# Optimization experiments

Measured on AMD Instinct MI355X. Metric: run time of the kernel, lower is better.

The kernel has to match this reference:

```python
import jax, jax.numpy as jnp
import numpy as np

B, T, D = 1, 2048, 2048
H, G, HD = 16, 4, 128          # num_heads, num_kv_groups, head_dim
GS = H // G                    # group_size
EPS = 1e-6


def rmsnorm(x, w):
    return x * jax.lax.rsqrt(jnp.mean(x * x, axis=-1, keepdims=True) + EPS) * w


def apply_rope(x, cos, sin, offset=0):
    # x: [B, heads, T, HD]; cos/sin: [max_seq, HD]
    t = x.shape[2]
    c = cos[offset:offset + t][None, None]  # [1,1,T,HD]
    s = sin[offset:offset + t][None, None]
    x1, x2 = x[..., : HD // 2], x[..., HD // 2:]
    rot = jnp.concatenate([-x2, x1], axis=-1)
    return x * c + rot * s


def setup_inputs() -> dict:
    key = jax.random.key(0)
    ks = jax.random.split(key, 8)
    x = jax.random.normal(ks[0], (B, T, D), dtype=jnp.float32)
    # causal mask: True = masked out
    mask = jnp.triu(jnp.ones((T, T), dtype=bool), k=1)[None, None]
    # RoPE tables (theta=10000), duplicated-halves layout
    inv_freq = 1.0 / (10000.0 ** (jnp.arange(0, HD, 2, dtype=jnp.float32) / HD))
    angles = jnp.arange(T, dtype=jnp.float32)[:, None] * inv_freq[None, :]  # [T, HD/2]
    angles = jnp.concatenate([angles, angles], axis=-1)                     # [T, HD]
    cos, sin = jnp.cos(angles), jnp.sin(angles)
    sc = 0.02
    Wq = jax.random.normal(ks[1], (H * HD, D), dtype=jnp.float32) * sc
    Wk = jax.random.normal(ks[2], (G * HD, D), dtype=jnp.float32) * sc
    Wv = jax.random.normal(ks[3], (G * HD, D), dtype=jnp.float32) * sc
    Wo = jax.random.normal(ks[4], (D, H * HD), dtype=jnp.float32) * sc
    q_norm_w = jnp.ones((H * HD,), dtype=jnp.float32)
    k_norm_w = jnp.ones((G * HD,), dtype=jnp.float32)
    return {"x": x, "mask": mask, "cos": cos, "sin": sin,
            "Wq": Wq, "Wk": Wk, "Wv": Wv, "Wo": Wo,
            "q_norm_w": q_norm_w, "k_norm_w": k_norm_w}


def reference(x, mask, cos, sin, Wq, Wk, Wv, Wo, q_norm_w, k_norm_w):
    b, t, _ = x.shape
    q = rmsnorm(x @ Wq.T, q_norm_w)   # [B,T,H*HD]
    k = rmsnorm(x @ Wk.T, k_norm_w)   # [B,T,G*HD]
    v = x @ Wv.T                      # [B,T,G*HD]
    q = q.reshape(b, t, H, HD).transpose(0, 2, 1, 3)   # [B,H,T,HD]
    k = k.reshape(b, t, G, HD).transpose(0, 2, 1, 3)   # [B,G,T,HD]
    v = v.reshape(b, t, G, HD).transpose(0, 2, 1, 3)
    q = apply_rope(q, cos, sin, offset=0)
    k = apply_rope(k, cos, sin, offset=0)
    # GQA: repeat_interleave KV heads to match query heads
    k = jnp.repeat(k, GS, axis=1)     # [B,H,T,HD]
    vr = jnp.repeat(v, GS, axis=1)
    q = q * (HD ** -0.5)
    scores = jnp.einsum('bhqd,bhkd->bhqk', q, k)        # [B,H,T,T]
    scores = jnp.where(mask, -jnp.inf, scores)
    attn = jax.nn.softmax(scores, axis=-1)
    ctx = jnp.einsum('bhqk,bhkd->bhqd', attn, vr)
    ctx = ctx.transpose(0, 2, 1, 3).reshape(b, t, H * HD)
    return ctx @ Wo.T                                   # [B,T,D]
```

## Files before the change

kernel.cpp:

```cpp
#include <hip/hip_runtime.h>

#define T_SEQ 2048
#define DMODEL 2048
#define NHEADS 16
#define NKV 4
#define HDIM 128
#define KVDIM (NKV*HDIM)
#define QKVN (DMODEL + 2*KVDIM)

typedef __bf16 bf16x8 __attribute__((ext_vector_type(8)));
typedef float f32x4 __attribute__((ext_vector_type(4)));
typedef unsigned short us8 __attribute__((ext_vector_type(8)));
typedef unsigned short ushort_t;

__device__ __forceinline__ ushort_t f2b(float f) {
    union { float f; unsigned u; } c; c.f = f;
    unsigned r = c.u + 0x7FFFu + ((c.u >> 16) & 1u);
    return (ushort_t)(r >> 16);
}
__device__ __forceinline__ float b2f(ushort_t b) {
    union { unsigned u; float f; } c; c.u = ((unsigned)b) << 16; return c.f;
}

#define GLDS(g, l) __builtin_amdgcn_global_load_lds( \
    (const __attribute__((address_space(1))) void*)(g), \
    (__attribute__((address_space(3))) void*)(l), 16, 0, 0)

__global__ __launch_bounds__(256) void cvt_kernel(const float* __restrict__ s,
                                                  ushort_t* __restrict__ d, int n) {
    int i = (blockIdx.x * 256 + threadIdx.x) * 4;
    if (i < n) {
        const float4 v = *(const float4*)(s + i);
        ushort4 o = make_ushort4(f2b(v.x), f2b(v.y), f2b(v.z), f2b(v.w));
        *(ushort4*)(d + i) = o;
    }
}

template<int MODE>
__global__ __launch_bounds__(256) void gemm_bt(
    const ushort_t* __restrict__ A, const ushort_t* __restrict__ B,
    ushort_t* __restrict__ Cb, float* __restrict__ Cf, ushort_t* __restrict__ VT,
    int M, int N, int K)
{
    __shared__ ushort_t As[128 * 64];
    __shared__ ushort_t Bs[128 * 64];
    const int tid = threadIdx.x;
    const int lane = tid & 63;
    const int wv = tid >> 6;
    const int wr = wv >> 1, wc = wv & 1;
    const int lrow = lane & 15, lhi = lane >> 4;
    const int m0 = blockIdx.y * 128, n0 = blockIdx.x * 128;

    f32x4 acc[4][4];
#pragma unroll
    for (int i = 0; i < 4; i++)
#pragma unroll
        for (int j = 0; j < 4; j++) acc[i][j] = f32x4{0.f, 0.f, 0.f, 0.f};

    const int srow = tid >> 3;
    const int scol = (tid & 7) * 8;

    for (int kt = 0; kt < K; kt += 64) {
        if (kt) __syncthreads();
#pragma unroll
        for (int r = 0; r < 4; ++r) {
            int row = srow + r * 32;
            GLDS(A + (size_t)(m0 + row) * K + kt + scol, As + row * 64 + scol);
            GLDS(B + (size_t)(n0 + row) * K + kt + scol, Bs + row * 64 + scol);
        }
        __syncthreads();
#pragma unroll
        for (int kk = 0; kk < 2; ++kk) {
            bf16x8 af[4], bfr[4];
#pragma unroll
            for (int i = 0; i < 4; i++)
                af[i] = *(const bf16x8*)(As + (wr * 64 + i * 16 + lrow) * 64 + kk * 32 + lhi * 8);
#pragma unroll
            for (int j = 0; j < 4; j++)
                bfr[j] = *(const bf16x8*)(Bs + (wc * 64 + j * 16 + lrow) * 64 + kk * 32 + lhi * 8);
#pragma unroll
            for (int i = 0; i < 4; i++)
#pragma unroll
                for (int j = 0; j < 4; j++)
                    acc[i][j] = __builtin_amdgcn_mfma_f32_16x16x32_bf16(af[i], bfr[j], acc[i][j], 0, 0, 0);
        }
    }
    if (MODE == 2 && n0 >= DMODEL + KVDIM) {
#pragma unroll
        for (int i = 0; i < 4; i++)
#pragma unroll
            for (int j = 0; j < 4; j++) {
                int col = n0 + wc * 64 + j * 16 + lrow - (DMODEL + KVDIM);
                int row0 = m0 + wr * 64 + i * 16 + lhi * 4;
                ushort4 pk = make_ushort4(f2b(acc[i][j][0]), f2b(acc[i][j][1]),
                                          f2b(acc[i][j][2]), f2b(acc[i][j][3]));
                *(ushort4*)(VT + (size_t)col * T_SEQ + row0) = pk;
            }
    } else {
#pragma unroll
        for (int i = 0; i < 4; i++)
#pragma unroll
            for (int j = 0; j < 4; j++)
#pragma unroll
                for (int e = 0; e < 4; e++) {
                    int row = m0 + wr * 64 + i * 16 + lhi * 4 + e;
                    int col = n0 + wc * 64 + j * 16 + lrow;
                    if (MODE == 1) Cf[(size_t)row * N + col] = acc[i][j][e];
                    else           Cb[(size_t)row * N + col] = f2b(acc[i][j][e]);
                }
    }
}

template<int DROW>
__global__ __launch_bounds__(256) void norm_rope(
    const ushort_t* __restrict__ src, int sld, int scol,
    const float* __restrict__ w,
    const float* __restrict__ cosT, const float* __restrict__ sinT,
    ushort_t* __restrict__ dst, int dld, float oscale)
{
    constexpr int PER = DROW / 256;
    __shared__ float rowbuf[DROW];
    __shared__ float red[4];
    const int tid = threadIdx.x;
    const int t = blockIdx.x;
    const ushort_t* rp = src + (size_t)t * sld + scol;
    const int e0 = tid * PER;

    float vals[PER];
    if constexpr (PER == 8) {
        us8 u = *(const us8*)(rp + e0);
#pragma unroll
        for (int p = 0; p < PER; p++) vals[p] = b2f(u[p]);
    } else {
        ushort2 u = *(const ushort2*)(rp + e0);
        vals[0] = b2f(u.x); vals[1] = b2f(u.y);
    }
    float ss = 0.f;
#pragma unroll
    for (int p = 0; p < PER; p++) { ss += vals[p] * vals[p]; rowbuf[e0 + p] = vals[p]; }
#pragma unroll
    for (int o = 32; o; o >>= 1) ss += __shfl_down(ss, o);
    if ((tid & 63) == 0) red[tid >> 6] = ss;
    __syncthreads();
    float rn = rsqrtf((red[0] + red[1] + red[2] + red[3]) / (float)DROW + 1e-6f);
#pragma unroll
    for (int p = 0; p < PER; p++) {
        int e = e0 + p, r = e & 127;
        float c = cosT[t * HDIM + r], s = sinT[t * HDIM + r];
        int pe = (r < 64) ? e + 64 : e - 64;
        float self = rowbuf[e] * rn * w[e];
        float part = rowbuf[pe] * rn * w[pe];
        float o = (r < 64) ? (self * c - part * s) : (self * c + part * s);
        dst[(size_t)t * dld + e] = f2b(o * oscale);
    }
}

__global__ __launch_bounds__(256) void fattn(
    const ushort_t* __restrict__ Q,
    const ushort_t* __restrict__ Kb,
    const ushort_t* __restrict__ VT,
    ushort_t* __restrict__ ctx)
{
    __shared__ ushort_t Ks[2][64 * 128];
    __shared__ ushort_t Vt[2][128 * 64];
    __shared__ ushort_t Pw[4][16 * 64];
    const int tid = threadIdx.x, lane = tid & 63, wv = tid >> 6;
    const int lrow = lane & 15, lhi = lane >> 4;
    const int h = blockIdx.x;
    const int qt = 31 - (int)blockIdx.y;
    const int g = h >> 2;
    const int q0 = qt * 64;

    const int srK = tid >> 4, scK = tid & 15;
    const int srV = tid >> 3, scV = tid & 7;

    bf16x8 qf[4];
    {
        int qr = q0 + wv * 16 + lrow;
#pragma unroll
        for (int ks = 0; ks < 4; ks++)
            qf[ks] = *(const bf16x8*)(Q + (size_t)qr * DMODEL + h * HDIM + ks * 32 + lhi * 8);
    }
    f32x4 of[8];
#pragma unroll
    for (int f = 0; f < 8; f++) of[f] = f32x4{0.f, 0.f, 0.f, 0.f};
    float m_[4], l_[4];
#pragma unroll
    for (int j = 0; j < 4; j++) { m_[j] = -1e30f; l_[j] = 0.f; }
    int myrow[4];
#pragma unroll
    for (int j = 0; j < 4; j++) myrow[j] = q0 + wv * 16 + lhi * 4 + j;

    auto stage = [&](int kt, int b) {
        const int k0 = kt * 64;
#pragma unroll
        for (int r = 0; r < 4; r++) {
            int row = srK + r * 16;
            int c = scK ^ (row & 7);
            GLDS(Kb + (size_t)(k0 + row) * KVDIM + g * HDIM + c * 8,
                 Ks[b] + row * 128 + scK * 8);
        }
#pragma unroll
        for (int r = 0; r < 4; r++) {
            int row = srV + r * 32;
            int c = scV ^ (row & 7);
            GLDS(VT + (size_t)(g * HDIM + row) * T_SEQ + k0 + c * 8,
                 Vt[b] + row * 64 + scV * 8);
        }
    };

    stage(0, 0);
    __syncthreads();
    int buf = 0;

    for (int kt = 0; kt <= qt; ++kt) {
        if (kt < qt) stage(kt + 1, buf ^ 1);
        const ushort_t* KsB = Ks[buf];
        const ushort_t* VtB = Vt[buf];
        const int k0 = kt * 64;

        f32x4 sf[4];
#pragma unroll
        for (int nf = 0; nf < 4; nf++) sf[nf] = f32x4{0.f, 0.f, 0.f, 0.f};
#pragma unroll
        for (int ks = 0; ks < 4; ks++) {
#pragma unroll
            for (int nf = 0; nf < 4; nf++) {
                bf16x8 kf = *(const bf16x8*)(KsB + (nf * 16 + lrow) * 128 +
                                             (((ks * 4 + lhi) ^ (lrow & 7)) << 3));
                sf[nf] = __builtin_amdgcn_mfma_f32_16x16x32_bf16(qf[ks], kf, sf[nf], 0, 0, 0);
            }
        }
#pragma unroll
        for (int nf = 0; nf < 4; nf++) {
            int key = k0 + nf * 16 + lrow;
#pragma unroll
            for (int j = 0; j < 4; j++)
                if (key > myrow[j]) sf[nf][j] = -1e30f;
        }
        float pf[4][4], sc[4];
#pragma unroll
        for (int j = 0; j < 4; j++) {
            float mx = fmaxf(fmaxf(sf[0][j], sf[1][j]), fmaxf(sf[2][j], sf[3][j]));
#pragma unroll
            for (int o = 1; o < 16; o <<= 1) mx = fmaxf(mx, __shfl_xor(mx, o));
            float mn = fmaxf(m_[j], mx);
            sc[j] = __expf(m_[j] - mn);
            m_[j] = mn;
        }
#pragma unroll
        for (int nf = 0; nf < 4; nf++)
#pragma unroll
            for (int j = 0; j < 4; j++) pf[nf][j] = __expf(sf[nf][j] - m_[j]);
#pragma unroll
        for (int j = 0; j < 4; j++) {
            float rs = pf[0][j] + pf[1][j] + pf[2][j] + pf[3][j];
#pragma unroll
            for (int o = 1; o < 16; o <<= 1) rs += __shfl_xor(rs, o);
            l_[j] = l_[j] * sc[j] + rs;
        }
#pragma unroll
        for (int f = 0; f < 8; f++)
#pragma unroll
            for (int j = 0; j < 4; j++) of[f][j] *= sc[j];
#pragma unroll
        for (int nf = 0; nf < 4; nf++)
#pragma unroll
            for (int j = 0; j < 4; j++) {
                int q = lhi * 4 + j;
                int cb = (nf * 16 + lrow) * 2;
                int cbp = cb ^ ((q & 7) << 4);
                Pw[wv][q * 64 + (cbp >> 1)] = f2b(pf[nf][j]);
            }
#pragma unroll
        for (int k2 = 0; k2 < 2; k2++) {
            bf16x8 pa = *(const bf16x8*)(Pw[wv] + lrow * 64 +
                                         (((k2 * 4 + lhi) ^ (lrow & 7)) << 3));
#pragma unroll
            for (int f = 0; f < 8; f++) {
                bf16x8 vf = *(const bf16x8*)(VtB + (f * 16 + lrow) * 64 +
                                             (((k2 * 4 + lhi) ^ (lrow & 7)) << 3));
                of[f] = __builtin_amdgcn_mfma_f32_16x16x32_bf16(pa, vf, of[f], 0, 0, 0);
            }
        }
        __syncthreads();
        buf ^= 1;
    }
#pragma unroll
    for (int f = 0; f < 8; f++)
#pragma unroll
        for (int j = 0; j < 4; j++) {
            float o = of[f][j] / l_[j];
            ctx[(size_t)myrow[j] * DMODEL + h * HDIM + f * 16 + lrow] = f2b(o);
        }
}

extern "C" void kernel_launch(void* const* d_in, const int* in_sizes, int n_in,
                              void* d_out, int out_size, void* d_ws, size_t ws_size,
                              hipStream_t stream)
{
    const float* x    = (const float*)d_in[0];
    const float* cosT = (const float*)d_in[2];
    const float* sinT = (const float*)d_in[3];
    const float* Wq   = (const float*)d_in[4];
    const float* Wk   = (const float*)d_in[5];
    const float* Wv   = (const float*)d_in[6];
    const float* Wo   = (const float*)d_in[7];
    const float* qw   = (const float*)d_in[8];
    const float* kw   = (const float*)d_in[9];
    float* out = (float*)d_out;

    char* ws = (char*)d_ws;
    size_t off = 0;
    auto alloc = [&](size_t bytes) -> char* {
        char* p = ws + off; off += (bytes + 255) & ~(size_t)255; return p;
    };
    ushort_t* xb    = (ushort_t*)alloc((size_t)T_SEQ * DMODEL * 2);
    ushort_t* wqkvb = (ushort_t*)alloc((size_t)QKVN * DMODEL * 2);
    ushort_t* wob   = (ushort_t*)alloc((size_t)DMODEL * DMODEL * 2);
    ushort_t* qkvb  = (ushort_t*)alloc((size_t)T_SEQ * QKVN * 2);
    ushort_t* qb    = (ushort_t*)alloc((size_t)T_SEQ * DMODEL * 2);
    ushort_t* kb    = (ushort_t*)alloc((size_t)T_SEQ * KVDIM * 2);
    ushort_t* ctxb  = (ushort_t*)alloc((size_t)T_SEQ * DMODEL * 2);
    ushort_t* vtb   = (ushort_t*)alloc((size_t)KVDIM * T_SEQ * 2);

    auto cvt = [&](const float* s, ushort_t* d, int n) {
        cvt_kernel<<<dim3((n / 4 + 255) / 256), dim3(256), 0, stream>>>(s, d, n);
    };
    cvt(x,  xb, T_SEQ * DMODEL);
    cvt(Wq, wqkvb, DMODEL * DMODEL);
    cvt(Wk, wqkvb + (size_t)DMODEL * DMODEL, KVDIM * DMODEL);
    cvt(Wv, wqkvb + (size_t)(DMODEL + KVDIM) * DMODEL, KVDIM * DMODEL);
    cvt(Wo, wob, DMODEL * DMODEL);

    gemm_bt<2><<<dim3(QKVN / 128, T_SEQ / 128), dim3(256), 0, stream>>>(
        xb, wqkvb, qkvb, nullptr, vtb, T_SEQ, QKVN, DMODEL);

    norm_rope<DMODEL><<<dim3(T_SEQ), dim3(256), 0, stream>>>(
        qkvb, QKVN, 0, qw, cosT, sinT, qb, DMODEL, 0.08838834764831843f);
    norm_rope<KVDIM><<<dim3(T_SEQ), dim3(256), 0, stream>>>(
        qkvb, QKVN, DMODEL, kw, cosT, sinT, kb, KVDIM, 1.0f);

    fattn<<<dim3(NHEADS, 32), dim3(256), 0, stream>>>(qb, kb, vtb, ctxb);

    gemm_bt<1><<<dim3(DMODEL / 128, T_SEQ / 128), dim3(256), 0, stream>>>(
        ctxb, wob, nullptr, out, nullptr, T_SEQ, DMODEL, DMODEL);
}
```

Baseline: 306.2 us.

## Fuse conversion and norm-rope launches; lazy softmax rescale in attention

Merges the five fp32-to-bf16 conversion launches into a single kernel and the two norm/rope launches into one 2D-grid kernel, cutting launch overhead and tail effects. In flash attention, the running max and rescale of the accumulators are updated only when some row's max grows by more than a threshold (wave-wide vote). The per-tile row-sum shuffle reduction is deferred to the epilogue. It also switches to the hardware bf16 conversion for P and the output. Lazy rescaling trades a bounded growth in exp values for fewer multiplies and exps.

```diff
diff --git a/kernel.cpp b/kernel.cpp
--- a/kernel.cpp
+++ b/kernel.cpp
@@ -18,6 +18,9 @@
     unsigned r = c.u + 0x7FFFu + ((c.u >> 16) & 1u);
     return (ushort_t)(r >> 16);
 }
+__device__ __forceinline__ ushort_t f2b_rn(float f) {
+    union { __bf16 h; ushort_t u; } c; c.h = (__bf16)f; return c.u;
+}
 __device__ __forceinline__ float b2f(ushort_t b) {
     union { unsigned u; float f; } c; c.u = ((unsigned)b) << 16; return c.f;
 }
@@ -26,14 +29,24 @@
     (const __attribute__((address_space(1))) void*)(g), \
     (__attribute__((address_space(3))) void*)(l), 16, 0, 0)
 
-__global__ __launch_bounds__(256) void cvt_kernel(const float* __restrict__ s,
-                                                  ushort_t* __restrict__ d, int n) {
-    int i = (blockIdx.x * 256 + threadIdx.x) * 4;
-    if (i < n) {
-        const float4 v = *(const float4*)(s + i);
-        ushort4 o = make_ushort4(f2b(v.x), f2b(v.y), f2b(v.z), f2b(v.w));
-        *(ushort4*)(d + i) = o;
-    }
+__global__ __launch_bounds__(256) void cvt5_kernel(
+    const float* __restrict__ s0, ushort_t* __restrict__ d0, int c0,
+    const float* __restrict__ s1, ushort_t* __restrict__ d1, int c1,
+    const float* __restrict__ s2, ushort_t* __restrict__ d2, int c2,
+    const float* __restrict__ s3, ushort_t* __restrict__ d3, int c3,
+    const float* __restrict__ s4, ushort_t* __restrict__ d4, int c4)
+{
+    int u = blockIdx.x * 256 + threadIdx.x;
+    const float* s; ushort_t* d; int off;
+    if      (u < c0) { s = s0; d = d0; off = u; }
+    else if (u < c1) { s = s1; d = d1; off = u - c0; }
+    else if (u < c2) { s = s2; d = d2; off = u - c1; }
+    else if (u < c3) { s = s3; d = d3; off = u - c2; }
+    else if (u < c4) { s = s4; d = d4; off = u - c3; }
+    else return;
+    const float4 v = *(const float4*)(s + off * 4);
+    ushort4 o = make_ushort4(f2b(v.x), f2b(v.y), f2b(v.z), f2b(v.w));
+    *(ushort4*)(d + off * 4) = o;
 }
 
 template<int MODE>
@@ -112,15 +125,14 @@
 }
 
 template<int DROW>
-__global__ __launch_bounds__(256) void norm_rope(
+__device__ __forceinline__ void norm_rope_body(
     const ushort_t* __restrict__ src, int sld, int scol,
     const float* __restrict__ w,
     const float* __restrict__ cosT, const float* __restrict__ sinT,
-    ushort_t* __restrict__ dst, int dld, float oscale)
+    ushort_t* __restrict__ dst, int dld, float oscale,
+    float* rowbuf, float* red)
 {
     constexpr int PER = DROW / 256;
-    __shared__ float rowbuf[DROW];
-    __shared__ float red[4];
     const int tid = threadIdx.x;
     const int t = blockIdx.x;
     const ushort_t* rp = src + (size_t)t * sld + scol;
@@ -153,6 +165,22 @@
         float o = (r < 64) ? (self * c - part * s) : (self * c + part * s);
         dst[(size_t)t * dld + e] = f2b(o * oscale);
     }
+}
+
+__global__ __launch_bounds__(256) void norm_rope_qk(
+    const ushort_t* __restrict__ qkv,
+    const float* __restrict__ qw, const float* __restrict__ kw,
+    const float* __restrict__ cosT, const float* __restrict__ sinT,
+    ushort_t* __restrict__ qb, ushort_t* __restrict__ kb)
+{
+    __shared__ float rowbuf[DMODEL];
+    __shared__ float red[4];
+    if (blockIdx.y == 0)
+        norm_rope_body<DMODEL>(qkv, QKVN, 0, qw, cosT, sinT, qb, DMODEL,
+                               0.08838834764831843f, rowbuf, red);
+    else
+        norm_rope_body<KVDIM>(qkv, QKVN, DMODEL, kw, cosT, sinT, kb, KVDIM,
+                              1.0f, rowbuf, red);
 }
 
 __global__ __launch_bounds__(256) void fattn(
@@ -238,31 +266,35 @@
             for (int j = 0; j < 4; j++)
                 if (key > myrow[j]) sf[nf][j] = -1e30f;
         }
-        float pf[4][4], sc[4];
+        float mx[4];
 #pragma unroll
         for (int j = 0; j < 4; j++) {
-            float mx = fmaxf(fmaxf(sf[0][j], sf[1][j]), fmaxf(sf[2][j], sf[3][j]));
-#pragma unroll
-            for (int o = 1; o < 16; o <<= 1) mx = fmaxf(mx, __shfl_xor(mx, o));
-            float mn = fmaxf(m_[j], mx);
-            sc[j] = __expf(m_[j] - mn);
-            m_[j] = mn;
-        }
+            float m2 = fmaxf(fmaxf(sf[0][j], sf[1][j]), fmaxf(sf[2][j], sf[3][j]));
+#pragma unroll
+            for (int o = 1; o < 16; o <<= 1) m2 = fmaxf(m2, __shfl_xor(m2, o));
+            mx[j] = m2;
+        }
+        float need = fmaxf(fmaxf(mx[0] - m_[0], mx[1] - m_[1]),
+                           fmaxf(mx[2] - m_[2], mx[3] - m_[3]));
+        if (!__all(need <= 8.0f)) {
+#pragma unroll
+            for (int j = 0; j < 4; j++) {
+                float mn = fmaxf(m_[j], mx[j]);
+                float sc = __expf(m_[j] - mn);
+                m_[j] = mn;
+                l_[j] *= sc;
+#pragma unroll
+                for (int f = 0; f < 8; f++) of[f][j] *= sc;
+            }
+        }
+        float pf[4][4];
 #pragma unroll
         for (int nf = 0; nf < 4; nf++)
 #pragma unroll
             for (int j = 0; j < 4; j++) pf[nf][j] = __expf(sf[nf][j] - m_[j]);
 #pragma unroll
-        for (int j = 0; j < 4; j++) {
-            float rs = pf[0][j] + pf[1][j] + pf[2][j] + pf[3][j];
-#pragma unroll
-            for (int o = 1; o < 16; o <<= 1) rs += __shfl_xor(rs, o);
-            l_[j] = l_[j] * sc[j] + rs;
-        }
-#pragma unroll
-        for (int f = 0; f < 8; f++)
-#pragma unroll
-            for (int j = 0; j < 4; j++) of[f][j] *= sc[j];
+        for (int j = 0; j < 4; j++)
+            l_[j] += (pf[0][j] + pf[1][j]) + (pf[2][j] + pf[3][j]);
 #pragma unroll
         for (int nf = 0; nf < 4; nf++)
 #pragma unroll
@@ -270,7 +302,7 @@
                 int q = lhi * 4 + j;
                 int cb = (nf * 16 + lrow) * 2;
                 int cbp = cb ^ ((q & 7) << 4);
-                Pw[wv][q * 64 + (cbp >> 1)] = f2b(pf[nf][j]);
+                Pw[wv][q * 64 + (cbp >> 1)] = f2b_rn(pf[nf][j]);
             }
 #pragma unroll
         for (int k2 = 0; k2 < 2; k2++) {
@@ -287,11 +319,16 @@
         buf ^= 1;
     }
 #pragma unroll
+    for (int j = 0; j < 4; j++) {
+#pragma unroll
+        for (int o = 1; o < 16; o <<= 1) l_[j] += __shfl_xor(l_[j], o);
+    }
+#pragma unroll
     for (int f = 0; f < 8; f++)
 #pragma unroll
         for (int j = 0; j < 4; j++) {
             float o = of[f][j] / l_[j];
-            ctx[(size_t)myrow[j] * DMODEL + h * HDIM + f * 16 + lrow] = f2b(o);
+            ctx[(size_t)myrow[j] * DMODEL + h * HDIM + f * 16 + lrow] = f2b_rn(o);
         }
 }
 
@@ -324,22 +361,24 @@
     ushort_t* ctxb  = (ushort_t*)alloc((size_t)T_SEQ * DMODEL * 2);
     ushort_t* vtb   = (ushort_t*)alloc((size_t)KVDIM * T_SEQ * 2);
 
-    auto cvt = [&](const float* s, ushort_t* d, int n) {
-        cvt_kernel<<<dim3((n / 4 + 255) / 256), dim3(256), 0, stream>>>(s, d, n);
-    };
-    cvt(x,  xb, T_SEQ * DMODEL);
-    cvt(Wq, wqkvb, DMODEL * DMODEL);
-    cvt(Wk, wqkvb + (size_t)DMODEL * DMODEL, KVDIM * DMODEL);
-    cvt(Wv, wqkvb + (size_t)(DMODEL + KVDIM) * DMODEL, KVDIM * DMODEL);
-    cvt(Wo, wob, DMODEL * DMODEL);
+    const int n_x  = T_SEQ * DMODEL / 4;
+    const int n_wq = DMODEL * DMODEL / 4;
+    const int n_wk = KVDIM * DMODEL / 4;
+    const int n_wv = KVDIM * DMODEL / 4;
+    const int n_wo = DMODEL * DMODEL / 4;
+    const int c0 = n_x, c1 = c0 + n_wq, c2 = c1 + n_wk, c3 = c2 + n_wv, c4 = c3 + n_wo;
+    cvt5_kernel<<<dim3((c4 + 255) / 256), dim3(256), 0, stream>>>(
+        x,  xb, c0,
+        Wq, wqkvb, c1,
+        Wk, wqkvb + (size_t)DMODEL * DMODEL, c2,
+        Wv, wqkvb + (size_t)(DMODEL + KVDIM) * DMODEL, c3,
+        Wo, wob, c4);
 
     gemm_bt<2><<<dim3(QKVN / 128, T_SEQ / 128), dim3(256), 0, stream>>>(
         xb, wqkvb, qkvb, nullptr, vtb, T_SEQ, QKVN, DMODEL);
 
-    norm_rope<DMODEL><<<dim3(T_SEQ), dim3(256), 0, stream>>>(
-        qkvb, QKVN, 0, qw, cosT, sinT, qb, DMODEL, 0.08838834764831843f);
-    norm_rope<KVDIM><<<dim3(T_SEQ), dim3(256), 0, stream>>>(
-        qkvb, QKVN, DMODEL, kw, cosT, sinT, kb, KVDIM, 1.0f);
+    norm_rope_qk<<<dim3(T_SEQ, 2), dim3(256), 0, stream>>>(
+        qkvb, qw, kw, cosT, sinT, qb, kb);
 
     fattn<<<dim3(NHEADS, 32), dim3(256), 0, stream>>>(qb, kb, vtb, ctxb);
 
```

Result: faster. 292.3 us (-4.5%).
